# Performance work log

Hardware: AMD Instinct MI355X
Metric: run time of the kernel (lower is better)

## Reference

```python
import jax, jax.numpy as jnp
import numpy as np

N = 50000          # nodes
E = 800000         # edges (avg degree 16)
IN_FEATS = 128
OUT_FEATS = 64
HEADS = 4
HID = HEADS * OUT_FEATS  # 256
NEG_SLOPE = 0.2          # PyG GATConv default
EPS = 1e-5               # BatchNorm eps


def setup_inputs() -> dict:
    key = jax.random.key(0)
    ks = jax.random.split(key, 8)
    x = jax.random.normal(ks[0], (N, IN_FEATS), dtype=jnp.float32)
    edge_index = jax.random.randint(ks[1], (2, E), 0, N, dtype=jnp.int32)
    edge_attr = jax.random.normal(ks[2], (E, 8), dtype=jnp.float32)  # unused (edge_dim=None)
    # GATConv params
    W_gat = jax.random.normal(ks[3], (IN_FEATS, HEADS, OUT_FEATS), jnp.float32) * (1.0 / np.sqrt(IN_FEATS))
    att_src = jax.random.normal(ks[4], (HEADS, OUT_FEATS), jnp.float32) * 0.1
    att_dst = jax.random.normal(ks[5], (HEADS, OUT_FEATS), jnp.float32) * 0.1
    bias_gat = jnp.zeros((HID,), jnp.float32)
    # BatchNorm1 + Linear + BatchNorm2 params
    bn1_gamma = jnp.ones((HID,), jnp.float32)
    bn1_beta = jnp.zeros((HID,), jnp.float32)
    W_lin = jax.random.normal(ks[6], (HID, OUT_FEATS), jnp.float32) * (1.0 / np.sqrt(HID))
    b_lin = jnp.zeros((OUT_FEATS,), jnp.float32)
    bn2_gamma = jnp.ones((OUT_FEATS,), jnp.float32)
    bn2_beta = jnp.zeros((OUT_FEATS,), jnp.float32)
    return dict(x=x, edge_attr=edge_attr, W_gat=W_gat, att_src=att_src, att_dst=att_dst,
                bias_gat=bias_gat, bn1_gamma=bn1_gamma, bn1_beta=bn1_beta,
                W_lin=W_lin, b_lin=b_lin, bn2_gamma=bn2_gamma, bn2_beta=bn2_beta,
                edge_index=edge_index)


def _batch_norm(h, gamma, beta):
    mu = h.mean(axis=0)
    var = h.var(axis=0)
    return (h - mu) * jax.lax.rsqrt(var + EPS) * gamma + beta


def reference(x, edge_attr, W_gat, att_src, att_dst, bias_gat,
              bn1_gamma, bn1_beta, W_lin, b_lin, bn2_gamma, bn2_beta,
              edge_index):
    # --- GATConv (add_self_loops=True, edge_attr ignored since edge_dim=None) ---
    loops = jnp.arange(N, dtype=edge_index.dtype)
    src = jnp.concatenate([edge_index[0], loops])  # [E+N]
    dst = jnp.concatenate([edge_index[1], loops])
    xh = jnp.einsum('ni,iho->nho', x, W_gat)       # [N, H, O]
    a_s = (xh * att_src).sum(-1)                   # [N, H]
    a_d = (xh * att_dst).sum(-1)                   # [N, H]
    e = a_s[src] + a_d[dst]                        # [E+N, H]
    e = jnp.where(e > 0, e, NEG_SLOPE * e)         # leaky_relu
    # segment softmax over destination node
    emax = jax.ops.segment_max(e, dst, num_segments=N)        # [N, H]
    ee = jnp.exp(e - emax[dst])
    denom = jax.ops.segment_sum(ee, dst, num_segments=N)
    alpha = ee / (denom[dst] + 1e-16)              # [E+N, H]
    msg = xh[src] * alpha[:, :, None]              # [E+N, H, O]
    out = jax.ops.segment_sum(msg, dst, num_segments=N)       # [N, H, O]
    h = out.reshape(N, HID) + bias_gat             # concat heads + bias
    # --- BatchNorm + ReLU + Linear + BatchNorm + ReLU ---
    h = jax.nn.relu(_batch_norm(h, bn1_gamma, bn1_beta))
    h = h @ W_lin + b_lin
    h = jax.nn.relu(_batch_norm(h, bn2_gamma, bn2_beta))
    return h
```

## Files before the change

kernel.cpp:

```cpp
#include <hip/hip_runtime.h>
#include <hip/hip_bf16.h>

#define IN_F 128
#define HID 256
#define OUT_F 64
#define NEG 0.2f
#define CAP 64

typedef __attribute__((ext_vector_type(8))) short bf16x8;
typedef __attribute__((ext_vector_type(4))) float f32x4;

__device__ __forceinline__ float lrelu(float v) { return v > 0.f ? v : NEG * v; }
__device__ __forceinline__ float bf2f(ushort u) { return __uint_as_float((uint)u << 16); }
__device__ __forceinline__ ushort f2bf(float f) {
    uint i = __float_as_uint(f);
    i += 0x7fffu + ((i >> 16) & 1u);
    return (ushort)(i >> 16);
}

__global__ void k_init(const float* __restrict__ Wg, const float* __restrict__ Wl,
                       ushort* __restrict__ Wgt, ushort* __restrict__ Wlt,
                       int* cnt, int Nn, float* stats) {
    int i = blockIdx.x * 256 + threadIdx.x;
    if (i < Nn) cnt[i] = 0;
    if (i < 640) stats[i] = 0.f;
    if (i < IN_F * HID) {
        int c = i >> 7, k = i & 127;
        Wgt[i] = f2bf(Wg[k * HID + c]);
    }
    if (i < OUT_F * HID) {
        int c = i >> 8, k = i & 255;
        Wlt[i] = f2bf(Wl[k * OUT_F + c]);
    }
}

__global__ __launch_bounds__(256) void k_scatter(const int* __restrict__ e_src,
                                                 const int* __restrict__ e_dst, int E,
                                                 int* __restrict__ cnt, int* __restrict__ bin) {
    int e = blockIdx.x * 256 + threadIdx.x;
    if (e >= E) return;
    int d = e_dst[e];
    int pos = atomicAdd(&cnt[d], 1);
    if (pos < CAP) bin[(size_t)d * CAP + pos] = e_src[e];
}

__global__ __launch_bounds__(256) void k_gemm(const float* __restrict__ x,
                                              const ushort* __restrict__ Wgt,
                                              const float* __restrict__ att_s,
                                              const float* __restrict__ att_d,
                                              ushort* __restrict__ xhb,
                                              float* __restrict__ a_s,
                                              float* __restrict__ a_d, int Nn) {
    __shared__ ushort Alds[64][136];
    int t = threadIdx.x;
    int w = t >> 6, lane = t & 63;
    int row0 = blockIdx.x * 64;

    for (int i = t; i < 2048; i += 256) {
        int r = i >> 5, c = i & 31;
        int gr = row0 + r;
        float4 v = make_float4(0.f, 0.f, 0.f, 0.f);
        if (gr < Nn) v = *(const float4*)(x + (size_t)gr * IN_F + c * 4);
        *(ushort4*)(&Alds[r][c * 4]) = make_ushort4(f2bf(v.x), f2bf(v.y), f2bf(v.z), f2bf(v.w));
    }

    int qw = lane >> 4, lr = lane & 15;
    bf16x8 bf[4][4];
#pragma unroll
    for (int ct = 0; ct < 4; ++ct)
#pragma unroll
        for (int kt = 0; kt < 4; ++kt) {
            int col = w * 64 + ct * 16 + lr;
            bf[ct][kt] = *(const bf16x8*)(Wgt + (size_t)col * IN_F + kt * 32 + qw * 8);
        }

    f32x4 zero = {0.f, 0.f, 0.f, 0.f};
    f32x4 acc[4][4];
#pragma unroll
    for (int rt = 0; rt < 4; ++rt)
#pragma unroll
        for (int ct = 0; ct < 4; ++ct) acc[rt][ct] = zero;

    __syncthreads();
#pragma unroll
    for (int kt = 0; kt < 4; ++kt) {
#pragma unroll
        for (int rt = 0; rt < 4; ++rt) {
            bf16x8 af = *(const bf16x8*)(&Alds[rt * 16 + lr][kt * 32 + qw * 8]);
#pragma unroll
            for (int ct = 0; ct < 4; ++ct)
                acc[rt][ct] = __builtin_amdgcn_mfma_f32_16x16x32_bf16(af, bf[ct][kt], acc[rt][ct], 0, 0, 0);
        }
    }

    float asv[4], adv[4];
#pragma unroll
    for (int ct = 0; ct < 4; ++ct) {
        asv[ct] = att_s[w * 64 + ct * 16 + lr];
        adv[ct] = att_d[w * 64 + ct * 16 + lr];
    }

#pragma unroll
    for (int rt = 0; rt < 4; ++rt)
#pragma unroll
        for (int r = 0; r < 4; ++r) {
            int row = row0 + rt * 16 + qw * 4 + r;
            float ss = 0.f, dd = 0.f;
#pragma unroll
            for (int ct = 0; ct < 4; ++ct) {
                float v = acc[rt][ct][r];
                ss += v * asv[ct];
                dd += v * adv[ct];
                if (row < Nn) xhb[(size_t)row * HID + w * 64 + ct * 16 + lr] = f2bf(v);
            }
#pragma unroll
            for (int off = 1; off < 16; off <<= 1) {
                ss += __shfl_xor(ss, off);
                dd += __shfl_xor(dd, off);
            }
            if (row < Nn && lr == 0) {
                a_s[row * 4 + w] = ss;
                a_d[row * 4 + w] = dd;
            }
        }
}

__global__ __launch_bounds__(256) void k_gat(const int* __restrict__ cnt,
                                             const int* __restrict__ bin,
                                             const ushort* __restrict__ xhb,
                                             const float* __restrict__ a_s,
                                             const float* __restrict__ a_d,
                                             const float* __restrict__ bias,
                                             ushort* __restrict__ hgb, int Nn) {
    int w = threadIdx.x >> 6, lane = threadIdx.x & 63;
    int i = blockIdx.x * 4 + w;
    if (i >= Nn) return;
    int deg = cnt[i]; if (deg > CAP) deg = CAP;
    const int* colp = bin + (size_t)i * CAP;
    int qq = lane >> 4;
    int r  = lane & 15;
    int h  = r >> 2;

    float adh = a_d[i * 4 + h];
    float ash = a_s[i * 4 + h];
    float ps = __expf(lrelu(ash + adh));

    float acc[16];
#pragma unroll
    for (int j = 0; j < 16; ++j) acc[j] = 0.f;

#define ACC8(U, P, B) \
    acc[B+0] += (P) * __uint_as_float((U).x << 16); \
    acc[B+1] += (P) * __uint_as_float((U).x & 0xffff0000u); \
    acc[B+2] += (P) * __uint_as_float((U).y << 16); \
    acc[B+3] += (P) * __uint_as_float((U).y & 0xffff0000u); \
    acc[B+4] += (P) * __uint_as_float((U).z << 16); \
    acc[B+5] += (P) * __uint_as_float((U).z & 0xffff0000u); \
    acc[B+6] += (P) * __uint_as_float((U).w << 16); \
    acc[B+7] += (P) * __uint_as_float((U).w & 0xffff0000u);

    if (qq == 0) {
        const ushort* rp = xhb + (size_t)i * HID + r * 16;
        uint4 s0 = *(const uint4*)rp;
        uint4 s1 = *(const uint4*)(rp + 8);
        ACC8(s0, ps, 0)
        ACC8(s1, ps, 8)
    }

    float dl = 0.f;
    for (int g = 0; g < deg; g += 8) {
        int sA = g + qq, sB = g + 4 + qq;
        bool vA = sA < deg, vB = sB < deg;
        int cA = colp[vA ? sA : deg - 1];
        int cB = colp[vB ? sB : deg - 1];
        float eA = a_s[cA * 4 + h] + adh;
        float eB = a_s[cB * 4 + h] + adh;
        const ushort* rpA = xhb + (size_t)cA * HID + r * 16;
        const ushort* rpB = xhb + (size_t)cB * HID + r * 16;
        uint4 a0 = *(const uint4*)rpA;
        uint4 a1 = *(const uint4*)(rpA + 8);
        uint4 b0 = *(const uint4*)rpB;
        uint4 b1 = *(const uint4*)(rpB + 8);
        float pA = vA ? __expf(lrelu(eA)) : 0.f;
        float pB = vB ? __expf(lrelu(eB)) : 0.f;
        dl += pA + pB;
        ACC8(a0, pA, 0)
        ACC8(a1, pA, 8)
        ACC8(b0, pB, 0)
        ACC8(b1, pB, 8)
    }
#undef ACC8

#pragma unroll
    for (int j = 0; j < 16; ++j) {
        acc[j] += __shfl_xor(acc[j], 16);
        acc[j] += __shfl_xor(acc[j], 32);
    }
    dl += __shfl_xor(dl, 16);
    dl += __shfl_xor(dl, 32);

    if (qq == 0) {
        float inv = 1.f / (dl + ps + 1e-16f);
        const float4* bp = (const float4*)(bias + r * 16);
        uint ow[8];
#pragma unroll
        for (int pquad = 0; pquad < 4; ++pquad) {
            float4 b4 = bp[pquad];
            float v0 = acc[pquad * 4 + 0] * inv + b4.x;
            float v1 = acc[pquad * 4 + 1] * inv + b4.y;
            float v2 = acc[pquad * 4 + 2] * inv + b4.z;
            float v3 = acc[pquad * 4 + 3] * inv + b4.w;
            ow[pquad * 2 + 0] = (uint)f2bf(v0) | ((uint)f2bf(v1) << 16);
            ow[pquad * 2 + 1] = (uint)f2bf(v2) | ((uint)f2bf(v3) << 16);
        }
        uint4* dst = (uint4*)(hgb + (size_t)i * HID + r * 16);
        dst[0] = make_uint4(ow[0], ow[1], ow[2], ow[3]);
        dst[1] = make_uint4(ow[4], ow[5], ow[6], ow[7]);
    }
}

__global__ __launch_bounds__(256) void k_bnstat1(const ushort* __restrict__ hgb, int Nn,
                                                 float* __restrict__ sums) {
    __shared__ float sbuf[512];
    int t = threadIdx.x;
    sbuf[t] = 0.f; sbuf[t + 256] = 0.f;
    __syncthreads();
    int c0 = (t & 31) * 8;
    float s[8] = {}, sq[8] = {};
    for (int row = blockIdx.x * 8 + (t >> 5); row < Nn; row += gridDim.x * 8) {
        uint4 u = *(const uint4*)(hgb + (size_t)row * HID + c0);
        uint uu[4] = {u.x, u.y, u.z, u.w};
#pragma unroll
        for (int p = 0; p < 4; ++p) {
            float v0 = __uint_as_float(uu[p] << 16);
            float v1 = __uint_as_float(uu[p] & 0xffff0000u);
            s[p * 2] += v0;  sq[p * 2] += v0 * v0;
            s[p * 2 + 1] += v1; sq[p * 2 + 1] += v1 * v1;
        }
    }
#pragma unroll
    for (int j = 0; j < 8; ++j) {
        atomicAdd(&sbuf[c0 + j], s[j]);
        atomicAdd(&sbuf[256 + c0 + j], sq[j]);
    }
    __syncthreads();
    atomicAdd(&sums[t], sbuf[t]);
    atomicAdd(&sums[256 + t], sbuf[t + 256]);
}

__global__ __launch_bounds__(256) void k_lin(const ushort* __restrict__ hgb,
                                             const float* __restrict__ bn1s, float Ninv,
                                             const float* __restrict__ g1, const float* __restrict__ b1,
                                             const ushort* __restrict__ Wlt,
                                             const float* __restrict__ bl,
                                             ushort* __restrict__ h2b,
                                             float* __restrict__ bn2s, int Nn) {
    __shared__ ushort Alds[128][264];
    __shared__ float sc1[256], sf1[256];
    __shared__ float sbuf2[128];
    int t = threadIdx.x;
    int w = t >> 6, lane = t & 63;
    int row0 = blockIdx.x * 128;

    {
        float mu = bn1s[t] * Ninv;
        float var = bn1s[256 + t] * Ninv - mu * mu;
        float a = g1[t] * rsqrtf(var + 1e-5f);
        sc1[t] = a; sf1[t] = b1[t] - mu * a;
    }
    if (t < 128) sbuf2[t] = 0.f;
    __syncthreads();

    for (int i = t; i < 4096; i += 256) {
        int rr = i >> 5, c8 = (i & 31) * 8;
        int gr = row0 + rr;
        ushort ob[8] = {0, 0, 0, 0, 0, 0, 0, 0};
        if (gr < Nn) {
            uint4 u = *(const uint4*)(hgb + (size_t)gr * HID + c8);
            uint uu[4] = {u.x, u.y, u.z, u.w};
#pragma unroll
            for (int p = 0; p < 4; ++p) {
                float v0 = __uint_as_float(uu[p] << 16);
                float v1 = __uint_as_float(uu[p] & 0xffff0000u);
                int cA = c8 + p * 2, cB = cA + 1;
                v0 = fmaxf(v0 * sc1[cA] + sf1[cA], 0.f);
                v1 = fmaxf(v1 * sc1[cB] + sf1[cB], 0.f);
                ob[p * 2] = f2bf(v0);
                ob[p * 2 + 1] = f2bf(v1);
            }
        }
        *(ushort4*)(&Alds[rr][c8]) = make_ushort4(ob[0], ob[1], ob[2], ob[3]);
        *(ushort4*)(&Alds[rr][c8 + 4]) = make_ushort4(ob[4], ob[5], ob[6], ob[7]);
    }
    __syncthreads();

    int qw = lane >> 4, lr = lane & 15;
    f32x4 zero = {0.f, 0.f, 0.f, 0.f};
    f32x4 acc[2][4];
#pragma unroll
    for (int a = 0; a < 2; ++a)
#pragma unroll
        for (int b = 0; b < 4; ++b) acc[a][b] = zero;

#pragma unroll
    for (int kt = 0; kt < 8; ++kt) {
        bf16x8 a0 = *(const bf16x8*)(&Alds[w * 32 + lr][kt * 32 + qw * 8]);
        bf16x8 a1 = *(const bf16x8*)(&Alds[w * 32 + 16 + lr][kt * 32 + qw * 8]);
#pragma unroll
        for (int ct = 0; ct < 4; ++ct) {
            bf16x8 b = *(const bf16x8*)(Wlt + (size_t)(ct * 16 + lr) * HID + kt * 32 + qw * 8);
            acc[0][ct] = __builtin_amdgcn_mfma_f32_16x16x32_bf16(a0, b, acc[0][ct], 0, 0, 0);
            acc[1][ct] = __builtin_amdgcn_mfma_f32_16x16x32_bf16(a1, b, acc[1][ct], 0, 0, 0);
        }
    }

#pragma unroll
    for (int ct = 0; ct < 4; ++ct) {
        float blc = bl[ct * 16 + lr];
        float s2 = 0.f, q2 = 0.f;
#pragma unroll
        for (int rt = 0; rt < 2; ++rt)
#pragma unroll
            for (int r = 0; r < 4; ++r) {
                int row = row0 + w * 32 + rt * 16 + qw * 4 + r;
                if (row < Nn) {
                    ushort u = f2bf(acc[rt][ct][r] + blc);
                    h2b[(size_t)row * OUT_F + ct * 16 + lr] = u;
                    float vr = bf2f(u);
                    s2 += vr; q2 += vr * vr;
                }
            }
        atomicAdd(&sbuf2[ct * 16 + lr], s2);
        atomicAdd(&sbuf2[64 + ct * 16 + lr], q2);
    }
    __syncthreads();
    if (t < 128) atomicAdd(&bn2s[t], sbuf2[t]);
}

__global__ __launch_bounds__(256) void k_out(const ushort* __restrict__ h2b,
                                             const float* __restrict__ bn2s, float Ninv,
                                             const float* __restrict__ g2, const float* __restrict__ b2,
                                             float* __restrict__ out, int Nn) {
    __shared__ float sc[64], sf[64];
    int t = threadIdx.x;
    if (t < 64) {
        float mu = bn2s[t] * Ninv;
        float var = bn2s[64 + t] * Ninv - mu * mu;
        float a = g2[t] * rsqrtf(var + 1e-5f);
        sc[t] = a; sf[t] = b2[t] - mu * a;
    }
    __syncthreads();
    int total8 = Nn * 8;
    for (int i = blockIdx.x * 256 + t; i < total8; i += gridDim.x * 256) {
        uint4 u = ((const uint4*)h2b)[i];
        int c0 = (i & 7) * 8;
        uint uu[4] = {u.x, u.y, u.z, u.w};
        float o[8];
#pragma unroll
        for (int p = 0; p < 4; ++p) {
            float v0 = __uint_as_float(uu[p] << 16);
            float v1 = __uint_as_float(uu[p] & 0xffff0000u);
            o[p * 2] = fmaxf(v0 * sc[c0 + p * 2] + sf[c0 + p * 2], 0.f);
            o[p * 2 + 1] = fmaxf(v1 * sc[c0 + p * 2 + 1] + sf[c0 + p * 2 + 1], 0.f);
        }
        float4* op = (float4*)(out + (size_t)i * 8);
        op[0] = make_float4(o[0], o[1], o[2], o[3]);
        op[1] = make_float4(o[4], o[5], o[6], o[7]);
    }
}

extern "C" void kernel_launch(void* const* d_in, const int* in_sizes, int n_in,
                              void* d_out, int out_size, void* d_ws, size_t ws_size,
                              hipStream_t stream) {
    const float* x     = (const float*)d_in[0];
    const float* Wg    = (const float*)d_in[2];
    const float* att_s = (const float*)d_in[3];
    const float* att_d = (const float*)d_in[4];
    const float* bias_g= (const float*)d_in[5];
    const float* g1    = (const float*)d_in[6];
    const float* b1    = (const float*)d_in[7];
    const float* Wl    = (const float*)d_in[8];
    const float* bl    = (const float*)d_in[9];
    const float* g2    = (const float*)d_in[10];
    const float* b2    = (const float*)d_in[11];
    const int*   ei    = (const int*)d_in[12];

    const int N = in_sizes[0] / IN_F;
    const int E = in_sizes[12] / 2;
    const int* e_src = ei;
    const int* e_dst = ei + E;
    const int NTILES = (N + 255) / 256;

    char* wsb = (char*)d_ws;
    size_t o = 0;
    auto take = [&](size_t bytes) -> void* {
        void* p = wsb + o;
        o = (o + bytes + 255) & ~(size_t)255;
        return p;
    };
    ushort* xhb    = (ushort*)take((size_t)N * HID * 2);
    ushort* hgb    = (ushort*)take((size_t)N * HID * 2);
    ushort* h2b    = (ushort*)take((size_t)N * OUT_F * 2);
    ushort* Wgt    = (ushort*)take((size_t)IN_F * HID * 2);
    ushort* Wlt    = (ushort*)take((size_t)OUT_F * HID * 2);
    float*  a_s    = (float*)take((size_t)N * 4 * 4);
    float*  a_d    = (float*)take((size_t)N * 4 * 4);
    int*    cnt    = (int*)take((size_t)N * 4);
    int*    bin    = (int*)take((size_t)N * CAP * 4);
    float*  stats  = (float*)take(1024 * 4);
    float* bn1s = stats;
    float* bn2s = stats + 512;

    float* out = (float*)d_out;
    float Ninv = 1.0f / (float)N;

    k_init<<<NTILES, 256, 0, stream>>>(Wg, Wl, Wgt, Wlt, cnt, N, stats);
    k_scatter<<<(E + 255) / 256, 256, 0, stream>>>(e_src, e_dst, E, cnt, bin);
    k_gemm<<<(N + 63) / 64, 256, 0, stream>>>(x, Wgt, att_s, att_d, xhb, a_s, a_d, N);
    k_gat<<<(N + 3) / 4, 256, 0, stream>>>(cnt, bin, xhb, a_s, a_d, bias_g, hgb, N);
    k_bnstat1<<<256, 256, 0, stream>>>(hgb, N, bn1s);
    k_lin<<<(N + 127) / 128, 256, 0, stream>>>(hgb, bn1s, Ninv, g1, b1, Wlt, bl, h2b, bn2s, N);
    k_out<<<1024, 256, 0, stream>>>(h2b, bn2s, Ninv, g2, b2, out, N);
}
```

Measured before the change: 200.0 us.

## Fuse edge scatter and GAT projection GEMM into one interleaved launch

Merges the edge-binning scatter kernel and the feature-projection GEMM kernel into a single launch. Block ids are interleaved so that one in five blocks runs a GEMM tile and the rest run scatter work. This lets the latency-bound atomic scatter overlap with the compute-bound GEMM and removes one launch boundary. In exchange, the scatter blocks carry the GEMM's shared-memory allocation, which may lower their occupancy.

```diff
diff --git a/kernel.cpp b/kernel.cpp
--- a/kernel.cpp
+++ b/kernel.cpp
@@ -34,27 +34,38 @@
     }
 }
 
-__global__ __launch_bounds__(256) void k_scatter(const int* __restrict__ e_src,
+__global__ __launch_bounds__(256) void k_gemm_sc(const float* __restrict__ x,
+                                                 const ushort* __restrict__ Wgt,
+                                                 const float* __restrict__ att_s,
+                                                 const float* __restrict__ att_d,
+                                                 const int* __restrict__ e_src,
                                                  const int* __restrict__ e_dst, int E,
-                                                 int* __restrict__ cnt, int* __restrict__ bin) {
-    int e = blockIdx.x * 256 + threadIdx.x;
-    if (e >= E) return;
-    int d = e_dst[e];
-    int pos = atomicAdd(&cnt[d], 1);
-    if (pos < CAP) bin[(size_t)d * CAP + pos] = e_src[e];
-}
-
-__global__ __launch_bounds__(256) void k_gemm(const float* __restrict__ x,
-                                              const ushort* __restrict__ Wgt,
-                                              const float* __restrict__ att_s,
-                                              const float* __restrict__ att_d,
-                                              ushort* __restrict__ xhb,
-                                              float* __restrict__ a_s,
-                                              float* __restrict__ a_d, int Nn) {
+                                                 int* __restrict__ cnt,
+                                                 int* __restrict__ bin,
+                                                 ushort* __restrict__ xhb,
+                                                 float* __restrict__ a_s,
+                                                 float* __restrict__ a_d,
+                                                 int Nn, int NG) {
     __shared__ ushort Alds[64][136];
+    int bid = blockIdx.x;
     int t = threadIdx.x;
+    int g = bid / 5;
+    bool is_gemm = (bid % 5 == 0) && (g < NG);
+
+    if (!is_gemm) {
+        int nGB = min((bid + 4) / 5, NG);
+        int sid = bid - nGB;
+        int e = sid * 256 + t;
+        if (e < E) {
+            int d = e_dst[e];
+            int pos = atomicAdd(&cnt[d], 1);
+            if (pos < CAP) bin[(size_t)d * CAP + pos] = e_src[e];
+        }
+        return;
+    }
+
     int w = t >> 6, lane = t & 63;
-    int row0 = blockIdx.x * 64;
+    int row0 = g * 64;
 
     for (int i = t; i < 2048; i += 256) {
         int r = i >> 5, c = i & 31;
@@ -390,6 +401,8 @@
     const int* e_src = ei;
     const int* e_dst = ei + E;
     const int NTILES = (N + 255) / 256;
+    const int NG = (N + 63) / 64;
+    const int NS = (E + 255) / 256;
 
     char* wsb = (char*)d_ws;
     size_t o = 0;
@@ -415,8 +428,8 @@
     float Ninv = 1.0f / (float)N;
 
     k_init<<<NTILES, 256, 0, stream>>>(Wg, Wl, Wgt, Wlt, cnt, N, stats);
-    k_scatter<<<(E + 255) / 256, 256, 0, stream>>>(e_src, e_dst, E, cnt, bin);
-    k_gemm<<<(N + 63) / 64, 256, 0, stream>>>(x, Wgt, att_s, att_d, xhb, a_s, a_d, N);
+    k_gemm_sc<<<NG + NS, 256, 0, stream>>>(x, Wgt, att_s, att_d, e_src, e_dst, E,
+                                           cnt, bin, xhb, a_s, a_d, N, NG);
     k_gat<<<(N + 3) / 4, 256, 0, stream>>>(cnt, bin, xhb, a_s, a_d, bias_g, hgb, N);
     k_bnstat1<<<256, 256, 0, stream>>>(hgb, N, bn1s);
     k_lin<<<(N + 127) / 128, 256, 0, stream>>>(hgb, bn1s, Ninv, g1, b1, Wlt, bl, h2b, bn2s, N);
```

Result: faster. 173.9 us (-13.1%).
